# Performance work log

Measured on AMD Instinct MI355X. Metric: run time of the kernel, lower is better.

Reference implementation:

```python
import jax, jax.numpy as jnp
import numpy as np

LAT_SIZE = 2048
BATCH = 4096


def cos_pos_encoding_1d(size, freq_div=2.0, sub_freq_max=4.0):
    freqs = list(range(1, int(size / freq_div)))
    spaces = [np.linspace(0, freq * 2 * np.pi, size) for freq in freqs]
    sub_freqs = [1.0 / float(i) for i in range(2, int(sub_freq_max))]
    sub_spaces = [np.linspace(i * freq * 2 * np.pi, (i + 1) * freq * 2 * np.pi, size)
                  for freq in sub_freqs for i in range(int(1 / freq))]
    spaces = spaces + sub_spaces
    cos = [np.cos(space) for space in spaces]
    return np.stack(cos).astype(np.float32)  # (n_freq, size)


def setup_inputs() -> dict:
    key = jax.random.key(0)
    k1, k2 = jax.random.split(key)
    cos_basis = jnp.asarray(cos_pos_encoding_1d(LAT_SIZE, 1, 8))  # (2074, 2048)
    n_freq = cos_basis.shape[0]
    x = jax.random.normal(k1, (BATCH, LAT_SIZE), dtype=jnp.float32)
    # nn.Linear default init: U(-1/sqrt(in), 1/sqrt(in))
    bound = 1.0 / np.sqrt(LAT_SIZE)
    W = jax.random.uniform(k2, (n_freq, LAT_SIZE), dtype=jnp.float32,
                           minval=-bound, maxval=bound)
    return {"x": x, "W": W, "cos_basis": cos_basis}


def reference(x, W, cos_basis):
    # x: (B, lat), W: (n_freq, lat), cos_basis: (n_freq, lat)
    x_freqs = x @ W.T                          # (B, n_freq)  -- to_freq_size
    # broadcast-mul + sum over freq dim == GEMM against fixed cosine basis
    out = x_freqs @ cos_basis                  # (B, lat)
    # global max-normalize (norm=True)
    return out / jnp.max(out)
```

## Files before the change

kernel.cpp:

```cpp
#include <hip/hip_runtime.h>
#include <hip/hip_bf16.h>
#include <cstdint>

#define BATCH 4096
#define LAT   2048
#define NFREQ 2074
#define KPAD  2112

typedef __bf16 bf16x8 __attribute__((ext_vector_type(8)));
typedef float  f32x4  __attribute__((ext_vector_type(4)));

__device__ __forceinline__ unsigned short f2bf(float f) {
    unsigned int u = __float_as_uint(f);
    u = (u + 0x7fffu + ((u >> 16) & 1u)) >> 16;
    return (unsigned short)u;
}

__device__ __forceinline__ void gload_lds16(const unsigned short* g, unsigned short* l) {
    __builtin_amdgcn_global_load_lds(
        (const __attribute__((address_space(1))) unsigned int*)g,
        (__attribute__((address_space(3))) unsigned int*)l,
        16, 0, 0);
}

__global__ void prep_kernel(const float* __restrict__ x,
                            const float* __restrict__ W,
                            const float* __restrict__ cb,
                            unsigned short* __restrict__ xb,
                            unsigned short* __restrict__ WT,
                            unsigned short* __restrict__ cosT,
                            float* __restrict__ maxp) {
    __shared__ float t[64][65];
    const int bid = blockIdx.x;
    const int tid = threadIdx.x;
    if (bid < 4096) {
        int i = bid * 256 + tid;
        const float4* x4 = (const float4*)x;
        float4 a = x4[2 * i];
        float4 b = x4[2 * i + 1];
        union { unsigned short us[8]; uint4 v; } p;
        p.us[0] = f2bf(a.x); p.us[1] = f2bf(a.y); p.us[2] = f2bf(a.z); p.us[3] = f2bf(a.w);
        p.us[4] = f2bf(b.x); p.us[5] = f2bf(b.y); p.us[6] = f2bf(b.z); p.us[7] = f2bf(b.w);
        ((uint4*)xb)[i] = p.v;
        if (i == 0) *maxp = -__builtin_inff();
        return;
    }
    int b2 = bid - 4096;
    const float* in     = (b2 < 1056) ? W  : cb;
    unsigned short* out = (b2 < 1056) ? WT : cosT;
    if (b2 >= 1056) b2 -= 1056;
    const int c0 = (b2 % 32) * 64;
    const int r0 = (b2 / 32) * 64;
    for (int i = tid; i < 4096; i += 256) {
        int rr = i >> 6, cc = i & 63;
        int r = r0 + rr;
        float v = (r < NFREQ) ? in[(size_t)r * LAT + c0 + cc] : 0.0f;
        t[rr][cc] = v;
    }
    __syncthreads();
    for (int i = tid; i < 4096; i += 256) {
        int cc = i >> 6, rr = i & 63;
        out[(size_t)(c0 + cc) * KPAD + (r0 + rr)] = f2bf(t[rr][cc]);
    }
}

template <int N, int K>
__global__ __launch_bounds__(256, 2)
void gemm1_kernel(const unsigned short* __restrict__ A,
                  const unsigned short* __restrict__ Bt,
                  unsigned short* __restrict__ C) {
    __shared__ alignas(16) unsigned short As[3][128 * 32];
    __shared__ alignas(16) unsigned short Bs[3][64 * 32];

    const int tid  = threadIdx.x;
    const int wave = tid >> 6;
    const int lane = tid & 63;
    const int wm   = (wave >> 1) * 64;
    const int wn   = (wave & 1) * 32;
    const int quad = lane >> 4;
    const int l16  = lane & 15;

    const int mBase = blockIdx.y * 128;
    const int nBase = blockIdx.x * 64;

    const int srow = lane >> 2;
    const int sk   = (lane & 3) * 8;

    const unsigned short* Ab1 = A  + (size_t)(mBase + (wave * 2 + 0) * 16 + srow) * K + sk;
    const unsigned short* Ab2 = A  + (size_t)(mBase + (wave * 2 + 1) * 16 + srow) * K + sk;
    const unsigned short* Bb1 = Bt + (size_t)(nBase + wave * 16 + srow) * K + sk;

    const int aoff1 = ((wave * 2 + 0) * 16) * 32;
    const int aoff2 = ((wave * 2 + 1) * 16) * 32;
    const int boff  = (wave * 16) * 32;

    constexpr int NIT = K / 32;
    gload_lds16(Ab1, &As[0][aoff1]);
    gload_lds16(Ab2, &As[0][aoff2]);
    gload_lds16(Bb1, &Bs[0][boff]);

    f32x4 acc[4][2] = {};
    int bc = 0;
    for (int j = 0; j < NIT; ++j) {
        const int bn = (bc == 2) ? 0 : bc + 1;
        if (j + 1 < NIT) {
            const int k0 = (j + 1) * 32;
            gload_lds16(Ab1 + k0, &As[bn][aoff1]);
            gload_lds16(Ab2 + k0, &As[bn][aoff2]);
            gload_lds16(Bb1 + k0, &Bs[bn][boff]);
            asm volatile("s_waitcnt vmcnt(3)\n\ts_barrier" ::: "memory");
        } else {
            asm volatile("s_waitcnt vmcnt(0)\n\ts_barrier" ::: "memory");
        }
        bf16x8 af[4], bfr[2];
#pragma unroll
        for (int mi = 0; mi < 4; ++mi)
            af[mi] = *(const bf16x8*)&As[bc][(wm + mi * 16 + l16) * 32 + quad * 8];
#pragma unroll
        for (int ni = 0; ni < 2; ++ni)
            bfr[ni] = *(const bf16x8*)&Bs[bc][(wn + ni * 16 + l16) * 32 + quad * 8];
#pragma unroll
        for (int mi = 0; mi < 4; ++mi)
#pragma unroll
            for (int ni = 0; ni < 2; ++ni)
                acc[mi][ni] = __builtin_amdgcn_mfma_f32_16x16x32_bf16(
                    af[mi], bfr[ni], acc[mi][ni], 0, 0, 0);
        bc = bn;
    }

#pragma unroll
    for (int mi = 0; mi < 4; ++mi)
#pragma unroll
        for (int ni = 0; ni < 2; ++ni) {
            int col = nBase + wn + ni * 16 + l16;
#pragma unroll
            for (int r = 0; r < 4; ++r) {
                int row = mBase + wm + mi * 16 + quad * 4 + r;
                C[(size_t)row * N + col] = f2bf(acc[mi][ni][r]);
            }
        }
}

template <int N, int K>
__global__ __launch_bounds__(512, 4)
void gemm2_kernel(const unsigned short* __restrict__ A,
                  const unsigned short* __restrict__ Bt,
                  float* __restrict__ C,
                  float* __restrict__ maxp) {
    __shared__ alignas(16) unsigned short As[3][128 * 32];
    __shared__ alignas(16) unsigned short Bs[3][128 * 32];
    __shared__ float redbuf[8];

    const int tid  = threadIdx.x;
    const int wave = tid >> 6;
    const int lane = tid & 63;
    const int wm   = (wave >> 2) * 64;
    const int wn   = (wave & 3) * 32;
    const int quad = lane >> 4;
    const int l16  = lane & 15;

    const int mBase = blockIdx.y * 128;
    const int nBase = blockIdx.x * 128;

    const int srow = lane >> 2;
    const int sk   = (lane & 3) * 8;

    const unsigned short* Ab1 = A  + (size_t)(mBase + wave * 16 + srow) * K + sk;
    const unsigned short* Bb1 = Bt + (size_t)(nBase + wave * 16 + srow) * K + sk;
    const int coff = (wave * 16) * 32;

    constexpr int NIT = K / 32;
    gload_lds16(Ab1, &As[0][coff]);
    gload_lds16(Bb1, &Bs[0][coff]);

    f32x4 acc[4][2] = {};
    int bc = 0;
    for (int j = 0; j < NIT; ++j) {
        const int bn = (bc == 2) ? 0 : bc + 1;
        if (j + 1 < NIT) {
            const int k0 = (j + 1) * 32;
            gload_lds16(Ab1 + k0, &As[bn][coff]);
            gload_lds16(Bb1 + k0, &Bs[bn][coff]);
            asm volatile("s_waitcnt vmcnt(2)\n\ts_barrier" ::: "memory");
        } else {
            asm volatile("s_waitcnt vmcnt(0)\n\ts_barrier" ::: "memory");
        }
        bf16x8 af[4], bfr[2];
#pragma unroll
        for (int mi = 0; mi < 4; ++mi)
            af[mi] = *(const bf16x8*)&As[bc][(wm + mi * 16 + l16) * 32 + quad * 8];
#pragma unroll
        for (int ni = 0; ni < 2; ++ni)
            bfr[ni] = *(const bf16x8*)&Bs[bc][(wn + ni * 16 + l16) * 32 + quad * 8];
#pragma unroll
        for (int mi = 0; mi < 4; ++mi)
#pragma unroll
            for (int ni = 0; ni < 2; ++ni)
                acc[mi][ni] = __builtin_amdgcn_mfma_f32_16x16x32_bf16(
                    af[mi], bfr[ni], acc[mi][ni], 0, 0, 0);
        bc = bn;
    }

    float vmax = -__builtin_inff();
#pragma unroll
    for (int mi = 0; mi < 4; ++mi)
#pragma unroll
        for (int ni = 0; ni < 2; ++ni) {
            int col = nBase + wn + ni * 16 + l16;
#pragma unroll
            for (int r = 0; r < 4; ++r) {
                int row = mBase + wm + mi * 16 + quad * 4 + r;
                float v = acc[mi][ni][r];
                C[(size_t)row * N + col] = v;
                vmax = fmaxf(vmax, v);
            }
        }
#pragma unroll
    for (int off = 32; off > 0; off >>= 1)
        vmax = fmaxf(vmax, __shfl_xor(vmax, off));
    if (lane == 0) redbuf[wave] = vmax;
    __syncthreads();
    if (tid == 0) {
        float m = redbuf[0];
#pragma unroll
        for (int w = 1; w < 8; ++w) m = fmaxf(m, redbuf[w]);
        if (m >= 0.0f) atomicMax((int*)maxp, __float_as_int(m));
        else           atomicMin((unsigned int*)maxp, __float_as_uint(m));
    }
}

__global__ void scale_kernel(float* __restrict__ out, const float* __restrict__ maxp) {
    int i = blockIdx.x * blockDim.x + threadIdx.x;
    float inv = 1.0f / (*maxp);
    float4* o4 = (float4*)out;
    float4 v = o4[i];
    v.x *= inv; v.y *= inv; v.z *= inv; v.w *= inv;
    o4[i] = v;
}

extern "C" void kernel_launch(void* const* d_in, const int* in_sizes, int n_in,
                              void* d_out, int out_size, void* d_ws, size_t ws_size,
                              hipStream_t stream) {
    const float* x  = (const float*)d_in[0];
    const float* W  = (const float*)d_in[1];
    const float* cb = (const float*)d_in[2];

    char* ws = (char*)d_ws;
    unsigned short* xb   = (unsigned short*)ws;
    unsigned short* WT   = (unsigned short*)(ws + (size_t)BATCH * LAT * 2);
    unsigned short* cosT = (unsigned short*)((char*)WT + (size_t)LAT * KPAD * 2);
    unsigned short* C1   = (unsigned short*)((char*)cosT + (size_t)LAT * KPAD * 2);
    float*          maxp = (float*)((char*)C1 + (size_t)LAT * LAT * 2);
    float*          out  = (float*)d_out;

    prep_kernel<<<4096 + 2 * 1056, 256, 0, stream>>>(x, W, cb, xb, WT, cosT, maxp);

    gemm1_kernel<LAT, KPAD>
        <<<dim3(LAT / 64, LAT / 128), 256, 0, stream>>>(cosT, WT, C1);

    gemm2_kernel<LAT, LAT>
        <<<dim3(LAT / 128, BATCH / 128), 512, 0, stream>>>(xb, C1, out, maxp);

    scale_kernel<<<(out_size / 4) / 256, 256, 0, stream>>>(out, maxp);
}
```

Before: 206.7 us.

## Fuse x conversion into gemm1, swizzle LDS, vectorize transpose, retile gemm1

The x fp32-to-bf16 conversion moves out of the prep kernel into extra blocks of the gemm1 launch, so it runs alongside the first GEMM. gemm1 is retiled to 128x128 tiles with 512 threads, matching gemm2. Both GEMMs get an XOR swizzle on the LDS k-chunk to cut bank conflicts. The prep transpose now uses float4 loads and ushort4 stores. The aim is to cut launch and serialization overhead and LDS conflicts, at the cost of mixing memory-bound blocks with compute blocks in one launch.

```diff
diff --git a/kernel.cpp b/kernel.cpp
--- a/kernel.cpp
+++ b/kernel.cpp
@@ -23,133 +23,69 @@
         16, 0, 0);
 }
 
-__global__ void prep_kernel(const float* __restrict__ x,
-                            const float* __restrict__ W,
+
+__global__ void prep_kernel(const float* __restrict__ W,
                             const float* __restrict__ cb,
-                            unsigned short* __restrict__ xb,
                             unsigned short* __restrict__ WT,
                             unsigned short* __restrict__ cosT,
                             float* __restrict__ maxp) {
     __shared__ float t[64][65];
     const int bid = blockIdx.x;
     const int tid = threadIdx.x;
-    if (bid < 4096) {
-        int i = bid * 256 + tid;
-        const float4* x4 = (const float4*)x;
-        float4 a = x4[2 * i];
-        float4 b = x4[2 * i + 1];
-        union { unsigned short us[8]; uint4 v; } p;
-        p.us[0] = f2bf(a.x); p.us[1] = f2bf(a.y); p.us[2] = f2bf(a.z); p.us[3] = f2bf(a.w);
-        p.us[4] = f2bf(b.x); p.us[5] = f2bf(b.y); p.us[6] = f2bf(b.z); p.us[7] = f2bf(b.w);
-        ((uint4*)xb)[i] = p.v;
-        if (i == 0) *maxp = -__builtin_inff();
-        return;
-    }
-    int b2 = bid - 4096;
-    const float* in     = (b2 < 1056) ? W  : cb;
-    unsigned short* out = (b2 < 1056) ? WT : cosT;
-    if (b2 >= 1056) b2 -= 1056;
+    if (bid == 0 && tid == 0) *maxp = -__builtin_inff();
+    const float* in     = (bid < 1056) ? W  : cb;
+    unsigned short* out = (bid < 1056) ? WT : cosT;
+    int b2 = (bid < 1056) ? bid : bid - 1056;
     const int c0 = (b2 % 32) * 64;
     const int r0 = (b2 / 32) * 64;
-    for (int i = tid; i < 4096; i += 256) {
-        int rr = i >> 6, cc = i & 63;
-        int r = r0 + rr;
-        float v = (r < NFREQ) ? in[(size_t)r * LAT + c0 + cc] : 0.0f;
-        t[rr][cc] = v;
+    for (int i = tid; i < 1024; i += 256) {
+        int rr = i >> 4;
+        int c4 = (i & 15) * 4;
+        int r  = r0 + rr;
+        float4 v;
+        if (r < NFREQ) v = *(const float4*)&in[(size_t)r * LAT + c0 + c4];
+        else           v = make_float4(0.f, 0.f, 0.f, 0.f);
+        t[rr][c4 + 0] = v.x; t[rr][c4 + 1] = v.y;
+        t[rr][c4 + 2] = v.z; t[rr][c4 + 3] = v.w;
     }
     __syncthreads();
-    for (int i = tid; i < 4096; i += 256) {
-        int cc = i >> 6, rr = i & 63;
-        out[(size_t)(c0 + cc) * KPAD + (r0 + rr)] = f2bf(t[rr][cc]);
+    for (int i = tid; i < 1024; i += 256) {
+        int cc = i >> 4;
+        int r4 = (i & 15) * 4;
+        ushort4 o;
+        o.x = f2bf(t[r4 + 0][cc]); o.y = f2bf(t[r4 + 1][cc]);
+        o.z = f2bf(t[r4 + 2][cc]); o.w = f2bf(t[r4 + 3][cc]);
+        *(ushort4*)&out[(size_t)(c0 + cc) * KPAD + r0 + r4] = o;
     }
 }
 
 template <int N, int K>
-__global__ __launch_bounds__(256, 2)
+__global__ __launch_bounds__(512, 4)
 void gemm1_kernel(const unsigned short* __restrict__ A,
                   const unsigned short* __restrict__ Bt,
-                  unsigned short* __restrict__ C) {
-    __shared__ alignas(16) unsigned short As[3][128 * 32];
-    __shared__ alignas(16) unsigned short Bs[3][64 * 32];
-
-    const int tid  = threadIdx.x;
-    const int wave = tid >> 6;
-    const int lane = tid & 63;
-    const int wm   = (wave >> 1) * 64;
-    const int wn   = (wave & 1) * 32;
-    const int quad = lane >> 4;
-    const int l16  = lane & 15;
-
-    const int mBase = blockIdx.y * 128;
-    const int nBase = blockIdx.x * 64;
-
-    const int srow = lane >> 2;
-    const int sk   = (lane & 3) * 8;
-
-    const unsigned short* Ab1 = A  + (size_t)(mBase + (wave * 2 + 0) * 16 + srow) * K + sk;
-    const unsigned short* Ab2 = A  + (size_t)(mBase + (wave * 2 + 1) * 16 + srow) * K + sk;
-    const unsigned short* Bb1 = Bt + (size_t)(nBase + wave * 16 + srow) * K + sk;
-
-    const int aoff1 = ((wave * 2 + 0) * 16) * 32;
-    const int aoff2 = ((wave * 2 + 1) * 16) * 32;
-    const int boff  = (wave * 16) * 32;
-
-    constexpr int NIT = K / 32;
-    gload_lds16(Ab1, &As[0][aoff1]);
-    gload_lds16(Ab2, &As[0][aoff2]);
-    gload_lds16(Bb1, &Bs[0][boff]);
-
-    f32x4 acc[4][2] = {};
-    int bc = 0;
-    for (int j = 0; j < NIT; ++j) {
-        const int bn = (bc == 2) ? 0 : bc + 1;
-        if (j + 1 < NIT) {
-            const int k0 = (j + 1) * 32;
-            gload_lds16(Ab1 + k0, &As[bn][aoff1]);
-            gload_lds16(Ab2 + k0, &As[bn][aoff2]);
-            gload_lds16(Bb1 + k0, &Bs[bn][boff]);
-            asm volatile("s_waitcnt vmcnt(3)\n\ts_barrier" ::: "memory");
-        } else {
-            asm volatile("s_waitcnt vmcnt(0)\n\ts_barrier" ::: "memory");
-        }
-        bf16x8 af[4], bfr[2];
-#pragma unroll
-        for (int mi = 0; mi < 4; ++mi)
-            af[mi] = *(const bf16x8*)&As[bc][(wm + mi * 16 + l16) * 32 + quad * 8];
-#pragma unroll
-        for (int ni = 0; ni < 2; ++ni)
-            bfr[ni] = *(const bf16x8*)&Bs[bc][(wn + ni * 16 + l16) * 32 + quad * 8];
-#pragma unroll
-        for (int mi = 0; mi < 4; ++mi)
-#pragma unroll
-            for (int ni = 0; ni < 2; ++ni)
-                acc[mi][ni] = __builtin_amdgcn_mfma_f32_16x16x32_bf16(
-                    af[mi], bfr[ni], acc[mi][ni], 0, 0, 0);
-        bc = bn;
-    }
-
-#pragma unroll
-    for (int mi = 0; mi < 4; ++mi)
-#pragma unroll
-        for (int ni = 0; ni < 2; ++ni) {
-            int col = nBase + wn + ni * 16 + l16;
-#pragma unroll
-            for (int r = 0; r < 4; ++r) {
-                int row = mBase + wm + mi * 16 + quad * 4 + r;
-                C[(size_t)row * N + col] = f2bf(acc[mi][ni][r]);
-            }
-        }
-}
-
-template <int N, int K>
-__global__ __launch_bounds__(512, 4)
-void gemm2_kernel(const unsigned short* __restrict__ A,
-                  const unsigned short* __restrict__ Bt,
-                  float* __restrict__ C,
-                  float* __restrict__ maxp) {
+                  unsigned short* __restrict__ C,
+                  const float* __restrict__ x,
+                  unsigned short* __restrict__ xb) {
+    if (blockIdx.y >= 16) {
+        const int cb  = (blockIdx.y - 16) * 16 + blockIdx.x;
+        const int tid = threadIdx.x;
+        const float4* x4 = (const float4*)x;
+        uint4* o4 = (uint4*)xb;
+        int i = cb * 512 + tid;
+#pragma unroll
+        for (int it = 0; it < 8; ++it, i += 131072) {
+            float4 a = x4[2 * i];
+            float4 b = x4[2 * i + 1];
+            union { unsigned short us[8]; uint4 v; } p;
+            p.us[0] = f2bf(a.x); p.us[1] = f2bf(a.y); p.us[2] = f2bf(a.z); p.us[3] = f2bf(a.w);
+            p.us[4] = f2bf(b.x); p.us[5] = f2bf(b.y); p.us[6] = f2bf(b.z); p.us[7] = f2bf(b.w);
+            o4[i] = p.v;
+        }
+        return;
+    }
+
     __shared__ alignas(16) unsigned short As[3][128 * 32];
     __shared__ alignas(16) unsigned short Bs[3][128 * 32];
-    __shared__ float redbuf[8];
 
     const int tid  = threadIdx.x;
     const int wave = tid >> 6;
@@ -163,11 +99,13 @@
     const int nBase = blockIdx.x * 128;
 
     const int srow = lane >> 2;
-    const int sk   = (lane & 3) * 8;
+    const int sk   = (((lane & 3) ^ ((srow >> 1) & 3))) * 8;
 
     const unsigned short* Ab1 = A  + (size_t)(mBase + wave * 16 + srow) * K + sk;
     const unsigned short* Bb1 = Bt + (size_t)(nBase + wave * 16 + srow) * K + sk;
     const int coff = (wave * 16) * 32;
+
+    const int pc = (quad ^ ((l16 >> 1) & 3)) * 8;
 
     constexpr int NIT = K / 32;
     gload_lds16(Ab1, &As[0][coff]);
@@ -188,10 +126,85 @@
         bf16x8 af[4], bfr[2];
 #pragma unroll
         for (int mi = 0; mi < 4; ++mi)
-            af[mi] = *(const bf16x8*)&As[bc][(wm + mi * 16 + l16) * 32 + quad * 8];
+            af[mi] = *(const bf16x8*)&As[bc][(wm + mi * 16 + l16) * 32 + pc];
 #pragma unroll
         for (int ni = 0; ni < 2; ++ni)
-            bfr[ni] = *(const bf16x8*)&Bs[bc][(wn + ni * 16 + l16) * 32 + quad * 8];
+            bfr[ni] = *(const bf16x8*)&Bs[bc][(wn + ni * 16 + l16) * 32 + pc];
+#pragma unroll
+        for (int mi = 0; mi < 4; ++mi)
+#pragma unroll
+            for (int ni = 0; ni < 2; ++ni)
+                acc[mi][ni] = __builtin_amdgcn_mfma_f32_16x16x32_bf16(
+                    af[mi], bfr[ni], acc[mi][ni], 0, 0, 0);
+        bc = bn;
+    }
+
+#pragma unroll
+    for (int mi = 0; mi < 4; ++mi)
+#pragma unroll
+        for (int ni = 0; ni < 2; ++ni) {
+            int col = nBase + wn + ni * 16 + l16;
+#pragma unroll
+            for (int r = 0; r < 4; ++r) {
+                int row = mBase + wm + mi * 16 + quad * 4 + r;
+                C[(size_t)row * N + col] = f2bf(acc[mi][ni][r]);
+            }
+        }
+}
+
+template <int N, int K>
+__global__ __launch_bounds__(512, 4)
+void gemm2_kernel(const unsigned short* __restrict__ A,
+                  const unsigned short* __restrict__ Bt,
+                  float* __restrict__ C,
+                  float* __restrict__ maxp) {
+    __shared__ alignas(16) unsigned short As[3][128 * 32];
+    __shared__ alignas(16) unsigned short Bs[3][128 * 32];
+    __shared__ float redbuf[8];
+
+    const int tid  = threadIdx.x;
+    const int wave = tid >> 6;
+    const int lane = tid & 63;
+    const int wm   = (wave >> 2) * 64;
+    const int wn   = (wave & 3) * 32;
+    const int quad = lane >> 4;
+    const int l16  = lane & 15;
+
+    const int mBase = blockIdx.y * 128;
+    const int nBase = blockIdx.x * 128;
+
+    const int srow = lane >> 2;
+    const int sk   = (((lane & 3) ^ ((srow >> 1) & 3))) * 8;
+
+    const unsigned short* Ab1 = A  + (size_t)(mBase + wave * 16 + srow) * K + sk;
+    const unsigned short* Bb1 = Bt + (size_t)(nBase + wave * 16 + srow) * K + sk;
+    const int coff = (wave * 16) * 32;
+
+    const int pc = (quad ^ ((l16 >> 1) & 3)) * 8;
+
+    constexpr int NIT = K / 32;
+    gload_lds16(Ab1, &As[0][coff]);
+    gload_lds16(Bb1, &Bs[0][coff]);
+
+    f32x4 acc[4][2] = {};
+    int bc = 0;
+    for (int j = 0; j < NIT; ++j) {
+        const int bn = (bc == 2) ? 0 : bc + 1;
+        if (j + 1 < NIT) {
+            const int k0 = (j + 1) * 32;
+            gload_lds16(Ab1 + k0, &As[bn][coff]);
+            gload_lds16(Bb1 + k0, &Bs[bn][coff]);
+            asm volatile("s_waitcnt vmcnt(2)\n\ts_barrier" ::: "memory");
+        } else {
+            asm volatile("s_waitcnt vmcnt(0)\n\ts_barrier" ::: "memory");
+        }
+        bf16x8 af[4], bfr[2];
+#pragma unroll
+        for (int mi = 0; mi < 4; ++mi)
+            af[mi] = *(const bf16x8*)&As[bc][(wm + mi * 16 + l16) * 32 + pc];
+#pragma unroll
+        for (int ni = 0; ni < 2; ++ni)
+            bfr[ni] = *(const bf16x8*)&Bs[bc][(wn + ni * 16 + l16) * 32 + pc];
 #pragma unroll
         for (int mi = 0; mi < 4; ++mi)
 #pragma unroll
@@ -253,10 +266,10 @@
     float*          maxp = (float*)((char*)C1 + (size_t)LAT * LAT * 2);
     float*          out  = (float*)d_out;
 
-    prep_kernel<<<4096 + 2 * 1056, 256, 0, stream>>>(x, W, cb, xb, WT, cosT, maxp);
+    prep_kernel<<<2 * 1056, 256, 0, stream>>>(W, cb, WT, cosT, maxp);
 
     gemm1_kernel<LAT, KPAD>
-        <<<dim3(LAT / 64, LAT / 128), 256, 0, stream>>>(cosT, WT, C1);
+        <<<dim3(16, 32), 512, 0, stream>>>(cosT, WT, C1, x, xb);
 
     gemm2_kernel<LAT, LAT>
         <<<dim3(LAT / 128, BATCH / 128), 512, 0, stream>>>(xb, C1, out, maxp);
```

New measurement: 191.6 us. 7.3% less time.
